# Optimization experiments

Hardware: AMD Instinct MI355X
Metric: run time of the kernel (lower is better)

Reference implementation:

```python
import jax, jax.numpy as jnp
import numpy as np

B, N, S, D1, D2 = 4, 16384, 4096, 128, 256
C_IN = D1 + D2  # 384
MLP = [256, 256]
EPS_BN = 1e-5


def setup_inputs() -> dict:
    key = jax.random.key(0)
    ks = jax.random.split(key, 16)
    inp = {
        "points_xyz1": jax.random.normal(ks[0], (B, N, 3), dtype=jnp.float32),
        "points_xyz2": jax.random.normal(ks[1], (B, S, 3), dtype=jnp.float32),
        "points_fea1": jax.random.normal(ks[2], (B, D1, N), dtype=jnp.float32),
        "points_fea2": jax.random.normal(ks[3], (B, D2, S), dtype=jnp.float32),
    }
    c_in = C_IN
    for i, c_out in enumerate(MLP):
        scale = 1.0 / np.sqrt(c_in)
        inp[f"W{i}"] = jax.random.uniform(ks[4 + 3 * i], (c_out, c_in), jnp.float32, -scale, scale)
        inp[f"b{i}"] = jax.random.uniform(ks[5 + 3 * i], (c_out,), jnp.float32, -scale, scale)
        inp[f"gamma{i}"] = jnp.ones((c_out,), jnp.float32)
        inp[f"beta{i}"] = jnp.zeros((c_out,), jnp.float32)
        c_in = c_out
    return inp


def _coordinate_distance(x1, x2):
    # squared euclidean distance matrix: (B,N,S)
    n1 = jnp.sum(x1 * x1, axis=-1, keepdims=True)          # (B,N,1)
    n2 = jnp.sum(x2 * x2, axis=-1, keepdims=True)          # (B,S,1)
    return n1 + jnp.swapaxes(n2, 1, 2) - 2.0 * jnp.einsum("bnc,bsc->bns", x1, x2)


def _conv_bn_relu(x, W, b, gamma, beta):
    # 1x1 conv: (B,Cin,N) -> (B,Cout,N), then BatchNorm1d (training stats) + ReLU
    y = jnp.einsum("oc,bcn->bon", W, x) + b[None, :, None]
    mean = jnp.mean(y, axis=(0, 2), keepdims=True)
    var = jnp.var(y, axis=(0, 2), keepdims=True)
    y = (y - mean) * jax.lax.rsqrt(var + EPS_BN)
    y = y * gamma[None, :, None] + beta[None, :, None]
    return jax.nn.relu(y)


def reference(points_xyz1, points_xyz2, points_fea1, points_fea2,
              W0, b0, gamma0, beta0, W1, b1, gamma1, beta1):
    dists = _coordinate_distance(points_xyz1[..., :3], points_xyz2[..., :3])  # (B,N,S)
    neg_d, idx = jax.lax.top_k(-dists, 3)                                     # 3 smallest
    d3 = -neg_d                                                               # (B,N,3)
    dist_recip = 1.0 / jnp.maximum(d3, 1e-8)
    weight = dist_recip / jnp.sum(dist_recip, axis=2, keepdims=True)          # (B,N,3)
    fea2t = jnp.swapaxes(points_fea2, 1, 2)                                   # (B,S,D2)
    gathered = fea2t[jnp.arange(B)[:, None, None], idx]                       # (B,N,3,D2)
    interp = jnp.sum(gathered * weight[..., None], axis=2)                    # (B,N,D2)
    new_fea = jnp.concatenate((points_fea1, jnp.swapaxes(interp, 1, 2)), axis=1)  # (B,D1+D2,N)
    new_fea = _conv_bn_relu(new_fea, W0, b0, gamma0, beta0)
    new_fea = _conv_bn_relu(new_fea, W1, b1, gamma1, beta1)
    return new_fea
```

## Files before the change

kernel.cpp:

```cpp
#include <hip/hip_runtime.h>
#include <math.h>

namespace {

constexpr int kB = 4;
constexpr int kN = 16384;
constexpr int kS = 4096;
constexpr int kD1 = 128;
constexpr int kD2 = 256;
constexpr int kCO = 256;
constexpr int kNCOL = kB * kN;
constexpr int kKX = kD1 + kD2;

constexpr size_t kOffAb0  = 262144;
constexpr size_t kOffX1p  = 266240;
constexpr size_t kOffPart = 33820672;
constexpr size_t kOffWbf  = 50597888;
constexpr size_t kOffW1bf = 50794496;

typedef __bf16 bf16x8 __attribute__((ext_vector_type(8)));
typedef float f32x4 __attribute__((ext_vector_type(4)));

__device__ __forceinline__ float bf2f(unsigned short u) {
  unsigned int x = ((unsigned int)u) << 16;
  float f;
  __builtin_memcpy(&f, &x, 4);
  return f;
}
__device__ __forceinline__ unsigned short f2bf(float f) {
  unsigned int x;
  __builtin_memcpy(&x, &f, 4);
  x += 0x7fffu + ((x >> 16) & 1u);
  return (unsigned short)(x >> 16);
}

__device__ __forceinline__ void cp16_async(const void* g, void* l) {
#if __has_builtin(__builtin_amdgcn_global_load_lds)
  __builtin_amdgcn_global_load_lds(
      (const __attribute__((address_space(1))) unsigned int*)g,
      (__attribute__((address_space(3))) unsigned int*)l, 16, 0, 0);
#else
  *(uint4*)l = *(const uint4*)g;
#endif
}


__global__ __launch_bounds__(256) void prep_kernel(
    const float* __restrict__ xyz2, float4* __restrict__ pts4,
    const float* __restrict__ fea2, float* __restrict__ fea2t,
    const float* __restrict__ fea1, unsigned short* __restrict__ XT,
    const float* __restrict__ W0, const float* __restrict__ W1,
    unsigned short* __restrict__ W0bf, unsigned short* __restrict__ W1bf) {
#pragma clang fp contract(off)
  __shared__ __align__(16) char lds_raw[33024];
  int bid = blockIdx.x;
  int t = threadIdx.x;
  if (bid >= 2112) {
    int gt = (bid - 2112) * 256 + t;
    int base = gt * 16;
    const float* src;
    unsigned short* dst;
    if (base < kCO * kKX) {
      src = W0 + base;
      dst = W0bf + base;
    } else {
      src = W1 + (base - kCO * kKX);
      dst = W1bf + (base - kCO * kKX);
    }
    float4 f0 = *(const float4*)(src);
    float4 f1 = *(const float4*)(src + 4);
    float4 f2 = *(const float4*)(src + 8);
    float4 f3 = *(const float4*)(src + 12);
    unsigned short h[16] = {f2bf(f0.x), f2bf(f0.y), f2bf(f0.z), f2bf(f0.w),
                            f2bf(f1.x), f2bf(f1.y), f2bf(f1.z), f2bf(f1.w),
                            f2bf(f2.x), f2bf(f2.y), f2bf(f2.z), f2bf(f2.w),
                            f2bf(f3.x), f2bf(f3.y), f2bf(f3.z), f2bf(f3.w)};
    ((uint4*)dst)[0] = ((uint4*)h)[0];
    ((uint4*)dst)[1] = ((uint4*)h)[1];
    return;
  }
  if (bid >= 1024 && bid < 1088) {
    int i = (bid - 1024) * 256 + t;
    float x = xyz2[i * 3 + 0];
    float y = xyz2[i * 3 + 1];
    float z = xyz2[i * 3 + 2];
    float4 p;
    p.w = (x * x + y * y) + z * z;
    p.x = x + x; p.y = y + y; p.z = z + z;
    pts4[i] = p;
    return;
  }
  if (bid < 1024) {
    float (*T)[65] = (float (*)[65])lds_raw;
    int s0 = (bid & 63) * 64;
    int c0 = ((bid >> 6) & 3) * 64;
    int b = bid >> 8;
    {
      int sl = t & 63, cg2 = t >> 6;
#pragma unroll
      for (int i = 0; i < 16; ++i) {
        int cl = cg2 * 16 + i;
        T[sl][cl] = fea2[((size_t)(b * kD2 + c0 + cl)) * kS + s0 + sl];
      }
    }
    __syncthreads();
    {
      int cl = t & 63, sg = t >> 6;
#pragma unroll
      for (int i = 0; i < 16; ++i) {
        int sl = sg * 16 + i;
        fea2t[((size_t)(b * kS + s0 + sl)) * kD2 + c0 + cl] = T[sl][cl];
      }
    }
    return;
  }
  {
    float (*T)[129] = (float (*)[129])lds_raw;
    int fb = bid - 1088;
    int n0 = (fb & 255) * 64;
    int b = fb >> 8;
    {
      int nl = t & 63, cg2 = t >> 6;
#pragma unroll
      for (int i = 0; i < 32; ++i) {
        int c = cg2 * 32 + i;
        T[nl][c] = fea1[((size_t)(b * kD1 + c)) * kN + n0 + nl];
      }
    }
    __syncthreads();
    {
      int nl = t >> 2, ch = t & 3;
      unsigned short h[32];
#pragma unroll
      for (int i = 0; i < 32; ++i) h[i] = f2bf(T[nl][ch * 32 + i]);
      uint4* dst = (uint4*)&XT[(size_t)(b * kN + n0 + nl) * kKX + ch * 32];
#pragma unroll
      for (int i = 0; i < 4; ++i) dst[i] = ((uint4*)h)[i];
    }
  }
}

__global__ __launch_bounds__(512) void knn_interp_kernel(
    const float* __restrict__ xyz1, const float4* __restrict__ pts4,
    const float* __restrict__ fea2t, unsigned short* __restrict__ XT) {
#pragma clang fp contract(off)
  __shared__ float cd[8][64][3];
  __shared__ int ci[8][64][3];
  __shared__ float wsh[3][64];
  __shared__ int ish[3][64];
  int tid = threadIdx.x;
  int q = tid & 63;
  int chunk = __builtin_amdgcn_readfirstlane(tid >> 6);
  int b = blockIdx.x >> 8;
  int n0 = (blockIdx.x & 255) * 64;
  int n = n0 + q;
  int qg = b * kN + n;

  const float* p1 = xyz1 + (size_t)qg * 3;
  float x = p1[0], y = p1[1], z = p1[2];
  float n1 = (x * x + y * y) + z * z;

  const float4* pp = pts4 + b * kS + chunk * 512;
  int sbase = chunk * 512;
  float d0v = 1e30f, d1v = 1e30f, d2v = 1e30f;
  int i0 = 0, i1 = 0, i2 = 0;
  for (int s = 0; s < 512; s += 4) {
    float4 P[4];
    P[0] = pp[s]; P[1] = pp[s + 1]; P[2] = pp[s + 2]; P[3] = pp[s + 3];
#pragma unroll
    for (int u = 0; u < 4; ++u) {
      float dot2 = (x * P[u].x + y * P[u].y) + z * P[u].z;
      float d = (n1 + P[u].w) - dot2;
      if (__ballot(d < d2v)) {
        int si = sbase + s + u;
        bool b0 = d < d0v, b1 = d < d1v, b2 = d < d2v;
        int i2n = b1 ? i1 : (b2 ? si : i2);
        int i1n = b0 ? i0 : (b1 ? si : i1);
        int i0n = b0 ? si : i0;
        d2v = __builtin_amdgcn_fmed3f(d1v, d, d2v);
        d1v = __builtin_amdgcn_fmed3f(d0v, d, d1v);
        d0v = fminf(d0v, d);
        i0 = i0n; i1 = i1n; i2 = i2n;
      }
    }
  }
  cd[chunk][q][0] = d0v; cd[chunk][q][1] = d1v; cd[chunk][q][2] = d2v;
  ci[chunk][q][0] = i0;  ci[chunk][q][1] = i1;  ci[chunk][q][2] = i2;
  __syncthreads();

  if (tid < 64) {
    float D0 = 1e30f, D1 = 1e30f, D2 = 1e30f;
    int I0 = -1, I1 = -1, I2 = -1;
    for (int c2 = 0; c2 < 8; ++c2) {
#pragma unroll
      for (int k = 0; k < 3; ++k) {
        float d = cd[c2][tid][k];
        int i = ci[c2][tid][k];
        bool q0 = (d < D0) || (d == D0 && i < I0);
        bool q1 = (d < D1) || (d == D1 && i < I1);
        bool q2 = (d < D2) || (d == D2 && i < I2);
        if (q0)      { D2 = D1; I2 = I1; D1 = D0; I1 = I0; D0 = d; I0 = i; }
        else if (q1) { D2 = D1; I2 = I1; D1 = d;  I1 = i; }
        else if (q2) { D2 = d;  I2 = i; }
      }
    }
    float r0 = 1.0f / fmaxf(D0, 1e-8f);
    float r1 = 1.0f / fmaxf(D1, 1e-8f);
    float r2 = 1.0f / fmaxf(D2, 1e-8f);
    float rs = (r0 + r1) + r2;
    wsh[0][tid] = r0 / rs; wsh[1][tid] = r1 / rs; wsh[2][tid] = r2 / rs;
    ish[0][tid] = I0; ish[1][tid] = I1; ish[2][tid] = I2;
  }
  __syncthreads();

  int gq = tid >> 3, l = tid & 7;
  float w0 = wsh[0][gq], w1 = wsh[1][gq], w2 = wsh[2][gq];
  int qg2 = b * kN + n0 + gq;
  const float* fb = fea2t + ((size_t)b * kS) * kD2;
  const float* g0p = fb + (size_t)ish[0][gq] * kD2;
  const float* g1p = fb + (size_t)ish[1][gq] * kD2;
  const float* g2p = fb + (size_t)ish[2][gq] * kD2;
  unsigned short* op = XT + (size_t)qg2 * kKX + kD1;
#pragma unroll
  for (int k = 0; k < 8; ++k) {
    int c = (l + 8 * k) * 4;
    float4 f0 = *(const float4*)(g0p + c);
    float4 f1 = *(const float4*)(g1p + c);
    float4 f2 = *(const float4*)(g2p + c);
    unsigned short h[4];
    h[0] = f2bf((w0 * f0.x + w1 * f1.x) + w2 * f2.x);
    h[1] = f2bf((w0 * f0.y + w1 * f1.y) + w2 * f2.y);
    h[2] = f2bf((w0 * f0.z + w1 * f1.z) + w2 * f2.z);
    h[3] = f2bf((w0 * f0.w + w1 * f1.w) + w2 * f2.w);
    *(uint2*)(op + c) = *(uint2*)h;
  }
}

__global__ __launch_bounds__(256) void gemm0t_kernel(
    const unsigned short* __restrict__ Wbf, const unsigned short* __restrict__ Bt,
    const float* __restrict__ bias, unsigned short* __restrict__ X1pre,
    float* __restrict__ partS, float* __restrict__ partQ) {
  constexpr int KDIM = kKX;
  __shared__ unsigned short smem[9216];
  unsigned short* As = smem;
  unsigned short* Bs = smem + 4096;
  __shared__ float psum[2][128], pq[2][128];
  int tid = threadIdx.x;
  int j0 = blockIdx.x * 128;
  int m0 = blockIdx.y * 128;
  int w = tid >> 6, lane = tid & 63;
  int wm = w & 1, wn = w >> 1;
  int quad = lane >> 4, l16 = lane & 15;
  int brow = tid >> 2, bch = tid & 3;
  int qs = bch ^ ((brow & 3) ^ ((brow >> 2) & 3));
  int qsw = quad ^ ((l16 & 3) ^ ((l16 >> 2) & 3));

  bf16x8 pone, pm;
#pragma unroll
  for (int i = 0; i < 8; ++i) { pone[i] = (__bf16)1.0f; pm[i] = (__bf16)(float)l16; }
  f32x4 zf = {};
  f32x4 dr = __builtin_amdgcn_mfma_f32_16x16x32_bf16(pm, pone, zf, 0, 0, 0);
  f32x4 dc = __builtin_amdgcn_mfma_f32_16x16x32_bf16(pone, pm, zf, 0, 0, 0);
  int rowv[4], colv[4];
#pragma unroll
  for (int r = 0; r < 4; ++r) {
    rowv[r] = (int)(dr[r] * (1.0f / 32.0f) + 0.5f);
    colv[r] = (int)(dc[r] * (1.0f / 32.0f) + 0.5f);
  }

  f32x4 acc[4][4] = {};
  for (int k0 = 0; k0 < KDIM; k0 += 32) {
    cp16_async(Bt + (size_t)(j0 + brow) * KDIM + k0 + qs * 8, &Bs[(size_t)tid * 8]);
    cp16_async(Bt + (size_t)(j0 + 64 + brow) * KDIM + k0 + qs * 8, &Bs[(size_t)(tid + 256) * 8]);
    cp16_async(Wbf + (size_t)(m0 + brow) * KDIM + k0 + qs * 8, &As[(size_t)tid * 8]);
    cp16_async(Wbf + (size_t)(m0 + 64 + brow) * KDIM + k0 + qs * 8, &As[(size_t)(tid + 256) * 8]);
    __syncthreads();
    bf16x8 af[4], bfr[4];
#pragma unroll
    for (int mt = 0; mt < 4; ++mt)
      af[mt] = *(const bf16x8*)(&As[(wm * 64 + mt * 16 + l16) * 32 + qsw * 8]);
#pragma unroll
    for (int nt = 0; nt < 4; ++nt)
      bfr[nt] = *(const bf16x8*)(&Bs[(wn * 64 + nt * 16 + l16) * 32 + qsw * 8]);
#pragma unroll
    for (int mt = 0; mt < 4; ++mt)
#pragma unroll
      for (int nt = 0; nt < 4; ++nt)
        acc[mt][nt] = __builtin_amdgcn_mfma_f32_16x16x32_bf16(af[mt], bfr[nt], acc[mt][nt], 0, 0, 0);
    __syncthreads();
  }

  uint2 h2[4][4];
#pragma unroll
  for (int mt = 0; mt < 4; ++mt) {
    int obase = m0 + wm * 64 + mt * 16 + rowv[0];
    float4 bv4 = *(const float4*)&bias[obase];
    float s4[4] = {0.f, 0.f, 0.f, 0.f}, q4[4] = {0.f, 0.f, 0.f, 0.f};
#pragma unroll
    for (int nt = 0; nt < 4; ++nt) {
      unsigned short hh[4];
#pragma unroll
      for (int r = 0; r < 4; ++r) {
        float v = acc[mt][nt][r] + ((const float*)&bv4)[r];
        s4[r] += v; q4[r] += v * v;
        hh[r] = f2bf(v);
      }
      h2[mt][nt] = *(uint2*)hh;
    }
#pragma unroll
    for (int r = 0; r < 4; ++r) {
      float s = s4[r], qq = q4[r];
#pragma unroll
      for (int d2 = 1; d2 < 16; d2 <<= 1) {
        s += __shfl_xor(s, d2, 64);
        qq += __shfl_xor(qq, d2, 64);
      }
      if (l16 == 0) {
        int ol = wm * 64 + mt * 16 + rowv[0] + r;
        psum[wn][ol] = s;
        pq[wn][ol] = qq;
      }
    }
  }

  unsigned short* T = smem + wm * 4608;
  int jr = lane >> 3, cc = lane & 7;
  if (wn == 0) {
#pragma unroll
    for (int mt = 0; mt < 4; ++mt)
#pragma unroll
      for (int nt = 0; nt < 4; ++nt)
        *(uint2*)&T[(nt * 16 + colv[0]) * 72 + mt * 16 + rowv[0]] = h2[mt][nt];
#pragma unroll
    for (int it = 0; it < 8; ++it) {
      int jl = it * 8 + jr;
      uint4 u = *(uint4*)&T[jl * 72 + cc * 8];
      *(uint4*)&X1pre[(size_t)(j0 + jl) * kCO + m0 + wm * 64 + cc * 8] = u;
    }
  }
  __syncthreads();
  if (wn == 1) {
#pragma unroll
    for (int mt = 0; mt < 4; ++mt)
#pragma unroll
      for (int nt = 0; nt < 4; ++nt)
        *(uint2*)&T[(nt * 16 + colv[0]) * 72 + mt * 16 + rowv[0]] = h2[mt][nt];
#pragma unroll
    for (int it = 0; it < 8; ++it) {
      int jl = it * 8 + jr;
      uint4 u = *(uint4*)&T[jl * 72 + cc * 8];
      *(uint4*)&X1pre[(size_t)(j0 + 64 + jl) * kCO + m0 + wm * 64 + cc * 8] = u;
    }
  }
  if (tid < 128) {
    float ss = psum[0][tid] + psum[1][tid];
    float qq = pq[0][tid] + pq[1][tid];
    partS[(size_t)(m0 + tid) * 512 + blockIdx.x] = ss;
    partQ[(size_t)(m0 + tid) * 512 + blockIdx.x] = qq;
  }
}

__global__ __launch_bounds__(64) void redstats_kernel(
    const float* __restrict__ pS, const float* __restrict__ pQ,
    const float* __restrict__ gamma, const float* __restrict__ beta,
    float* __restrict__ ab) {
  int o = blockIdx.x, t = threadIdx.x;
  float s = 0.f, q = 0.f;
  for (int i = t; i < 512; i += 64) {
    s += pS[(size_t)o * 512 + i];
    q += pQ[(size_t)o * 512 + i];
  }
#pragma unroll
  for (int d = 1; d < 64; d <<= 1) {
    s += __shfl_xor(s, d, 64);
    q += __shfl_xor(q, d, 64);
  }
  if (t == 0) {
    float m = s * (1.0f / 65536.f);
    float var = q * (1.0f / 65536.f) - m * m;
    float rsq = 1.0f / sqrtf(var + 1e-5f);
    float a = gamma[o] * rsq;
    ab[o] = a;
    ab[kCO + o] = beta[o] - m * a;
  }
}

__global__ __launch_bounds__(256) void gemm1f_kernel(
    const unsigned short* __restrict__ Wbf, const unsigned short* __restrict__ Xp,
    const float* __restrict__ bias, const float* __restrict__ ab0,
    float* __restrict__ out, float* __restrict__ partS, float* __restrict__ partQ) {
  constexpr int KDIM = kCO;
  __shared__ unsigned short As[4096];
  __shared__ unsigned short Bs[4096];
  __shared__ float Acf[256], Ccf[256];
  __shared__ float psum[2][128], pq[2][128];
  int tid = threadIdx.x;
  int j0 = blockIdx.x * 128;
  int m0 = blockIdx.y * 128;
  int w = tid >> 6, lane = tid & 63;
  int wm = w & 1, wn = w >> 1;
  int quad = lane >> 4, l16 = lane & 15;
  int brow = tid >> 2, bch = tid & 3;
  int qs = bch ^ ((brow & 3) ^ ((brow >> 2) & 3));
  int qsw = quad ^ ((l16 & 3) ^ ((l16 >> 2) & 3));

  if (tid < 256) { Acf[tid] = ab0[tid]; Ccf[tid] = ab0[kCO + tid]; }

  bf16x8 pone, pm;
#pragma unroll
  for (int i = 0; i < 8; ++i) { pone[i] = (__bf16)1.0f; pm[i] = (__bf16)(float)l16; }
  f32x4 zf = {};
  f32x4 dr = __builtin_amdgcn_mfma_f32_16x16x32_bf16(pm, pone, zf, 0, 0, 0);
  f32x4 dc = __builtin_amdgcn_mfma_f32_16x16x32_bf16(pone, pm, zf, 0, 0, 0);
  int rowv[4], colv[4];
#pragma unroll
  for (int r = 0; r < 4; ++r) {
    rowv[r] = (int)(dr[r] * (1.0f / 32.0f) + 0.5f);
    colv[r] = (int)(dc[r] * (1.0f / 32.0f) + 0.5f);
  }
  __syncthreads();

  f32x4 acc[4][4] = {};
  for (int k0 = 0; k0 < KDIM; k0 += 32) {
    {
      int cb = k0 + qs * 8;
      float4 a0 = *(const float4*)&Acf[cb];
      float4 a1 = *(const float4*)&Acf[cb + 4];
      float4 c0 = *(const float4*)&Ccf[cb];
      float4 c1 = *(const float4*)&Ccf[cb + 4];
#pragma unroll
      for (int h = 0; h < 2; ++h) {
        uint4 raw = *(const uint4*)(Xp + (size_t)(j0 + h * 64 + brow) * kCO + cb);
        const unsigned short* rs = (const unsigned short*)&raw;
        unsigned short o8[8];
        o8[0] = f2bf(fmaxf(fmaf(a0.x, bf2f(rs[0]), c0.x), 0.f));
        o8[1] = f2bf(fmaxf(fmaf(a0.y, bf2f(rs[1]), c0.y), 0.f));
        o8[2] = f2bf(fmaxf(fmaf(a0.z, bf2f(rs[2]), c0.z), 0.f));
        o8[3] = f2bf(fmaxf(fmaf(a0.w, bf2f(rs[3]), c0.w), 0.f));
        o8[4] = f2bf(fmaxf(fmaf(a1.x, bf2f(rs[4]), c1.x), 0.f));
        o8[5] = f2bf(fmaxf(fmaf(a1.y, bf2f(rs[5]), c1.y), 0.f));
        o8[6] = f2bf(fmaxf(fmaf(a1.z, bf2f(rs[6]), c1.z), 0.f));
        o8[7] = f2bf(fmaxf(fmaf(a1.w, bf2f(rs[7]), c1.w), 0.f));
        *(uint4*)&Bs[(size_t)(tid + h * 256) * 8] = *(uint4*)o8;
      }
    }
    cp16_async(Wbf + (size_t)(m0 + brow) * KDIM + k0 + qs * 8, &As[(size_t)tid * 8]);
    cp16_async(Wbf + (size_t)(m0 + 64 + brow) * KDIM + k0 + qs * 8, &As[(size_t)(tid + 256) * 8]);
    __syncthreads();
    bf16x8 af[4], bfr[4];
#pragma unroll
    for (int mt = 0; mt < 4; ++mt)
      af[mt] = *(const bf16x8*)(&As[(wm * 64 + mt * 16 + l16) * 32 + qsw * 8]);
#pragma unroll
    for (int nt = 0; nt < 4; ++nt)
      bfr[nt] = *(const bf16x8*)(&Bs[(wn * 64 + nt * 16 + l16) * 32 + qsw * 8]);
#pragma unroll
    for (int mt = 0; mt < 4; ++mt)
#pragma unroll
      for (int nt = 0; nt < 4; ++nt)
        acc[mt][nt] = __builtin_amdgcn_mfma_f32_16x16x32_bf16(af[mt], bfr[nt], acc[mt][nt], 0, 0, 0);
    __syncthreads();
  }

#pragma unroll
  for (int mt = 0; mt < 4; ++mt) {
#pragma unroll
    for (int r = 0; r < 4; ++r) {
      int ol = wm * 64 + mt * 16 + rowv[r];
      int o = m0 + ol;
      float bv = bias[o];
      float s = 0.f, qq = 0.f;
#pragma unroll
      for (int nt = 0; nt < 4; ++nt) {
        int j = j0 + wn * 64 + nt * 16 + colv[r];
        float v = acc[mt][nt][r] + bv;
        s += v; qq += v * v;
        int bb = j >> 14, nn = j & (kN - 1);
        out[((size_t)(bb * kCO + o)) * kN + nn] = v;
      }
#pragma unroll
      for (int d2 = 1; d2 < 16; d2 <<= 1) {
        s += __shfl_xor(s, d2, 64);
        qq += __shfl_xor(qq, d2, 64);
      }
      if (l16 == 0) {
        psum[wn][ol] = s;
        pq[wn][ol] = qq;
      }
    }
  }
  __syncthreads();
  if (tid < 128) {
    float ss = psum[0][tid] + psum[1][tid];
    float qq = pq[0][tid] + pq[1][tid];
    partS[(size_t)(m0 + tid) * 512 + blockIdx.x] = ss;
    partQ[(size_t)(m0 + tid) * 512 + blockIdx.x] = qq;
  }
}

__global__ __launch_bounds__(256) void finalf_kernel(
    float* __restrict__ Y, const float* __restrict__ pS,
    const float* __restrict__ pQ, const float* __restrict__ gamma,
    const float* __restrict__ beta) {
  __shared__ float sw[4], qw[4], coef[2];
  size_t base = (size_t)blockIdx.x * 1024;
  int o = (int)((base >> 14) & (kCO - 1));
  int tid = threadIdx.x;
  float s = pS[(size_t)o * 512 + tid] + pS[(size_t)o * 512 + 256 + tid];
  float q = pQ[(size_t)o * 512 + tid] + pQ[(size_t)o * 512 + 256 + tid];
#pragma unroll
  for (int d = 1; d < 64; d <<= 1) {
    s += __shfl_xor(s, d, 64);
    q += __shfl_xor(q, d, 64);
  }
  if ((tid & 63) == 0) { sw[tid >> 6] = s; qw[tid >> 6] = q; }
  __syncthreads();
  if (tid == 0) {
    float st = (sw[0] + sw[1]) + (sw[2] + sw[3]);
    float qt = (qw[0] + qw[1]) + (qw[2] + qw[3]);
    float m = st * (1.0f / 65536.f);
    float var = qt * (1.0f / 65536.f) - m * m;
    float rsq = 1.0f / sqrtf(var + 1e-5f);
    float a = gamma[o] * rsq;
    coef[0] = a;
    coef[1] = beta[o] - m * a;
  }
  __syncthreads();
  float a = coef[0], c = coef[1];
  float4 u = *(float4*)(Y + base + tid * 4);
  float* t = (float*)&u;
#pragma unroll
  for (int k = 0; k < 4; ++k) t[k] = fmaxf(fmaf(a, t[k], c), 0.0f);
  *(float4*)(Y + base + tid * 4) = u;
}

}

extern "C" void kernel_launch(void* const* d_in, const int* in_sizes, int n_in,
                              void* d_out, int out_size, void* d_ws, size_t ws_size,
                              hipStream_t stream) {
  const float* xyz1 = (const float*)d_in[0];
  const float* xyz2 = (const float*)d_in[1];
  const float* fea1 = (const float*)d_in[2];
  const float* fea2 = (const float*)d_in[3];
  const float* W0 = (const float*)d_in[4];
  const float* b0 = (const float*)d_in[5];
  const float* g0 = (const float*)d_in[6];
  const float* be0 = (const float*)d_in[7];
  const float* W1 = (const float*)d_in[8];
  const float* b1 = (const float*)d_in[9];
  const float* g1 = (const float*)d_in[10];
  const float* be1 = (const float*)d_in[11];
  float* out = (float*)d_out;

  char* ws = (char*)d_ws;
  float4* pts4 = (float4*)ws;
  float* ab0 = (float*)(ws + kOffAb0);
  unsigned short* X1pre = (unsigned short*)(ws + kOffX1p);
  float* partS = (float*)(ws + kOffPart);
  float* partQ = (float*)(ws + kOffPart + 524288);
  float* fea2t = (float*)(ws + kOffPart);
  unsigned short* W0bf = (unsigned short*)(ws + kOffWbf);
  unsigned short* W1bf = (unsigned short*)(ws + kOffW1bf);
  unsigned short* XT = (unsigned short*)d_out;

  if (ws_size < kOffW1bf + (size_t)kCO * kCO * 2) return;

  prep_kernel<<<2152, 256, 0, stream>>>(xyz2, pts4, fea2, fea2t, fea1, XT,
                                        W0, W1, W0bf, W1bf);
  knn_interp_kernel<<<kNCOL / 64, 512, 0, stream>>>(xyz1, pts4, fea2t, XT);
  gemm0t_kernel<<<dim3(kNCOL / 128, kCO / 128), 256, 0, stream>>>(W0bf, XT, b0, X1pre, partS, partQ);
  redstats_kernel<<<kCO, 64, 0, stream>>>(partS, partQ, g0, be0, ab0);
  gemm1f_kernel<<<dim3(kNCOL / 128, kCO / 128), 256, 0, stream>>>(W1bf, X1pre, b1, ab0, out, partS, partQ);
  finalf_kernel<<<kCO * kNCOL / (256 * 4), 256, 0, stream>>>(out, partS, partQ, g1, be1);
}
```

Measured before the change: 337.7 us.

## Double-buffer LDS tiles in both GEMM kernels to overlap loads with MFMA

Both GEMM kernels now use two LDS buffers. The next K-slice of weights and activations is issued (async copy, or the fused BN+ReLU staging in gemm1) before the MFMAs on the current slice, so each iteration has one barrier instead of two. This is meant to hide global-load latency behind the matrix work. LDS use per block rises to 32 KB, which may lower occupancy. The prefetch in gemm1 is synchronous register loads, so its overlap depends on how the compiler schedules them.

```diff
diff --git a/kernel.cpp b/kernel.cpp
--- a/kernel.cpp
+++ b/kernel.cpp
@@ -241,9 +241,7 @@
     const float* __restrict__ bias, unsigned short* __restrict__ X1pre,
     float* __restrict__ partS, float* __restrict__ partQ) {
   constexpr int KDIM = kKX;
-  __shared__ unsigned short smem[9216];
-  unsigned short* As = smem;
-  unsigned short* Bs = smem + 4096;
+  __shared__ unsigned short smem[16384];
   __shared__ float psum[2][128], pq[2][128];
   int tid = threadIdx.x;
   int j0 = blockIdx.x * 128;
@@ -268,13 +266,26 @@
     colv[r] = (int)(dc[r] * (1.0f / 32.0f) + 0.5f);
   }
 
+  cp16_async(Wbf + (size_t)(m0 + brow) * KDIM + qs * 8, &smem[(size_t)tid * 8]);
+  cp16_async(Wbf + (size_t)(m0 + 64 + brow) * KDIM + qs * 8, &smem[(size_t)(tid + 256) * 8]);
+  cp16_async(Bt + (size_t)(j0 + brow) * KDIM + qs * 8, &smem[4096 + (size_t)tid * 8]);
+  cp16_async(Bt + (size_t)(j0 + 64 + brow) * KDIM + qs * 8, &smem[4096 + (size_t)(tid + 256) * 8]);
+  __syncthreads();
+
   f32x4 acc[4][4] = {};
+  int cur = 0;
   for (int k0 = 0; k0 < KDIM; k0 += 32) {
-    cp16_async(Bt + (size_t)(j0 + brow) * KDIM + k0 + qs * 8, &Bs[(size_t)tid * 8]);
-    cp16_async(Bt + (size_t)(j0 + 64 + brow) * KDIM + k0 + qs * 8, &Bs[(size_t)(tid + 256) * 8]);
-    cp16_async(Wbf + (size_t)(m0 + brow) * KDIM + k0 + qs * 8, &As[(size_t)tid * 8]);
-    cp16_async(Wbf + (size_t)(m0 + 64 + brow) * KDIM + k0 + qs * 8, &As[(size_t)(tid + 256) * 8]);
-    __syncthreads();
+    unsigned short* As = smem + cur * 8192;
+    unsigned short* Bs = As + 4096;
+    int kn = k0 + 32;
+    if (kn < KDIM) {
+      unsigned short* An = smem + (cur ^ 1) * 8192;
+      unsigned short* Bn = An + 4096;
+      cp16_async(Wbf + (size_t)(m0 + brow) * KDIM + kn + qs * 8, &An[(size_t)tid * 8]);
+      cp16_async(Wbf + (size_t)(m0 + 64 + brow) * KDIM + kn + qs * 8, &An[(size_t)(tid + 256) * 8]);
+      cp16_async(Bt + (size_t)(j0 + brow) * KDIM + kn + qs * 8, &Bn[(size_t)tid * 8]);
+      cp16_async(Bt + (size_t)(j0 + 64 + brow) * KDIM + kn + qs * 8, &Bn[(size_t)(tid + 256) * 8]);
+    }
     bf16x8 af[4], bfr[4];
 #pragma unroll
     for (int mt = 0; mt < 4; ++mt)
@@ -288,6 +299,7 @@
       for (int nt = 0; nt < 4; ++nt)
         acc[mt][nt] = __builtin_amdgcn_mfma_f32_16x16x32_bf16(af[mt], bfr[nt], acc[mt][nt], 0, 0, 0);
     __syncthreads();
+    cur ^= 1;
   }
 
   uint2 h2[4][4];
@@ -390,8 +402,7 @@
     const float* __restrict__ bias, const float* __restrict__ ab0,
     float* __restrict__ out, float* __restrict__ partS, float* __restrict__ partQ) {
   constexpr int KDIM = kCO;
-  __shared__ unsigned short As[4096];
-  __shared__ unsigned short Bs[4096];
+  __shared__ unsigned short smem[16384];
   __shared__ float Acf[256], Ccf[256];
   __shared__ float psum[2][128], pq[2][128];
   int tid = threadIdx.x;
@@ -420,33 +431,46 @@
   }
   __syncthreads();
 
+  auto stageB = [&](int kk, unsigned short* Bsd) {
+    int cb = kk + qs * 8;
+    float4 a0 = *(const float4*)&Acf[cb];
+    float4 a1 = *(const float4*)&Acf[cb + 4];
+    float4 c0 = *(const float4*)&Ccf[cb];
+    float4 c1 = *(const float4*)&Ccf[cb + 4];
+#pragma unroll
+    for (int h = 0; h < 2; ++h) {
+      uint4 raw = *(const uint4*)(Xp + (size_t)(j0 + h * 64 + brow) * kCO + cb);
+      const unsigned short* rs = (const unsigned short*)&raw;
+      unsigned short o8[8];
+      o8[0] = f2bf(fmaxf(fmaf(a0.x, bf2f(rs[0]), c0.x), 0.f));
+      o8[1] = f2bf(fmaxf(fmaf(a0.y, bf2f(rs[1]), c0.y), 0.f));
+      o8[2] = f2bf(fmaxf(fmaf(a0.z, bf2f(rs[2]), c0.z), 0.f));
+      o8[3] = f2bf(fmaxf(fmaf(a0.w, bf2f(rs[3]), c0.w), 0.f));
+      o8[4] = f2bf(fmaxf(fmaf(a1.x, bf2f(rs[4]), c1.x), 0.f));
+      o8[5] = f2bf(fmaxf(fmaf(a1.y, bf2f(rs[5]), c1.y), 0.f));
+      o8[6] = f2bf(fmaxf(fmaf(a1.z, bf2f(rs[6]), c1.z), 0.f));
+      o8[7] = f2bf(fmaxf(fmaf(a1.w, bf2f(rs[7]), c1.w), 0.f));
+      *(uint4*)&Bsd[(size_t)(tid + h * 256) * 8] = *(uint4*)o8;
+    }
+  };
+
+  cp16_async(Wbf + (size_t)(m0 + brow) * KDIM + qs * 8, &smem[(size_t)tid * 8]);
+  cp16_async(Wbf + (size_t)(m0 + 64 + brow) * KDIM + qs * 8, &smem[(size_t)(tid + 256) * 8]);
+  stageB(0, smem + 4096);
+  __syncthreads();
+
   f32x4 acc[4][4] = {};
+  int cur = 0;
   for (int k0 = 0; k0 < KDIM; k0 += 32) {
-    {
-      int cb = k0 + qs * 8;
-      float4 a0 = *(const float4*)&Acf[cb];
-      float4 a1 = *(const float4*)&Acf[cb + 4];
-      float4 c0 = *(const float4*)&Ccf[cb];
-      float4 c1 = *(const float4*)&Ccf[cb + 4];
-#pragma unroll
-      for (int h = 0; h < 2; ++h) {
-        uint4 raw = *(const uint4*)(Xp + (size_t)(j0 + h * 64 + brow) * kCO + cb);
-        const unsigned short* rs = (const unsigned short*)&raw;
-        unsigned short o8[8];
-        o8[0] = f2bf(fmaxf(fmaf(a0.x, bf2f(rs[0]), c0.x), 0.f));
-        o8[1] = f2bf(fmaxf(fmaf(a0.y, bf2f(rs[1]), c0.y), 0.f));
-        o8[2] = f2bf(fmaxf(fmaf(a0.z, bf2f(rs[2]), c0.z), 0.f));
-        o8[3] = f2bf(fmaxf(fmaf(a0.w, bf2f(rs[3]), c0.w), 0.f));
-        o8[4] = f2bf(fmaxf(fmaf(a1.x, bf2f(rs[4]), c1.x), 0.f));
-        o8[5] = f2bf(fmaxf(fmaf(a1.y, bf2f(rs[5]), c1.y), 0.f));
-        o8[6] = f2bf(fmaxf(fmaf(a1.z, bf2f(rs[6]), c1.z), 0.f));
-        o8[7] = f2bf(fmaxf(fmaf(a1.w, bf2f(rs[7]), c1.w), 0.f));
-        *(uint4*)&Bs[(size_t)(tid + h * 256) * 8] = *(uint4*)o8;
-      }
-    }
-    cp16_async(Wbf + (size_t)(m0 + brow) * KDIM + k0 + qs * 8, &As[(size_t)tid * 8]);
-    cp16_async(Wbf + (size_t)(m0 + 64 + brow) * KDIM + k0 + qs * 8, &As[(size_t)(tid + 256) * 8]);
-    __syncthreads();
+    unsigned short* As = smem + cur * 8192;
+    unsigned short* Bs = As + 4096;
+    int kn = k0 + 32;
+    if (kn < KDIM) {
+      unsigned short* An = smem + (cur ^ 1) * 8192;
+      cp16_async(Wbf + (size_t)(m0 + brow) * KDIM + kn + qs * 8, &An[(size_t)tid * 8]);
+      cp16_async(Wbf + (size_t)(m0 + 64 + brow) * KDIM + kn + qs * 8, &An[(size_t)(tid + 256) * 8]);
+      stageB(kn, An + 4096);
+    }
     bf16x8 af[4], bfr[4];
 #pragma unroll
     for (int mt = 0; mt < 4; ++mt)
@@ -460,6 +484,7 @@
       for (int nt = 0; nt < 4; ++nt)
         acc[mt][nt] = __builtin_amdgcn_mfma_f32_16x16x32_bf16(af[mt], bfr[nt], acc[mt][nt], 0, 0, 0);
     __syncthreads();
+    cur ^= 1;
   }
 
 #pragma unroll
```

New measurement: 335.7 us. No clear change (-0.6%).
